# Performance work log

Hardware: AMD Instinct MI355X
Metric: run time of the kernel (lower is better)

The kernel has to match this reference:

```python
import math
import jax, jax.numpy as jnp
import numpy as np

B, C, T = 8, 512, 1024
H = 8
HD = C // H  # 64
CLIP = 4
COUT = 512


def setup_inputs() -> dict:
    key = jax.random.key(0)
    ks = jax.random.split(key, 12)
    s_qkv = math.sqrt(6.0 / (C + C))  # xavier_uniform for 1x1 conv
    queries = jax.random.normal(ks[0], (B, C, T), dtype=jnp.float32)
    Wq = jax.random.uniform(ks[1], (C, C), jnp.float32, -s_qkv, s_qkv)
    bq = jnp.zeros((C,), jnp.float32)
    Wk = jax.random.uniform(ks[2], (C, C), jnp.float32, -s_qkv, s_qkv)
    bk = jnp.zeros((C,), jnp.float32)
    Wv = jax.random.uniform(ks[3], (C, C), jnp.float32, -s_qkv, s_qkv)
    bv = jnp.zeros((C,), jnp.float32)
    Wp = jax.random.normal(ks[4], (COUT, C), jnp.float32) * (1.0 / math.sqrt(C))
    bp = jnp.zeros((COUT,), jnp.float32)
    w_std = HD ** (-0.5)
    wK = jax.random.normal(ks[5], (1, 2 * CLIP + 1, HD), jnp.float32) * w_std
    wV = jax.random.normal(ks[6], (1, 2 * CLIP + 1, HD), jnp.float32) * w_std
    return {"queries": queries, "Wq": Wq, "bq": bq, "Wk": Wk, "bk": bk,
            "Wv": Wv, "bv": bv, "Wp": Wp, "bp": bp, "wK": wK, "wV": wV}


def _get_relative_embedding(w, length):
    # w: [1, 2*CLIP+1, HD] -> [1, 2*length-1, HD]
    emb_len = 2 * length - 1
    p = max(emb_len - 2 * CLIP - 1, 0)
    pc, pf = (p + 1) // 2, p // 2  # ceil, floor of p/2
    w = jnp.pad(w, ((0, 0), (pc, pf), (0, 0)))
    idx = max(CLIP + 1 - length, 0)
    return w[:, idx:idx + emb_len]


def _rel_to_abs(x):
    # x: [B, H, L, 2L-1] -> [B, H, L, L]  (pad/shift trick)
    b, h, L, _ = x.shape
    x = jnp.pad(x, ((0, 0), (0, 0), (0, 0), (0, 1)))           # [b,h,L,2L]
    x = x.reshape(b, h, L * 2 * L)
    x = jnp.pad(x, ((0, 0), (0, 0), (0, L - 1)))
    x = x.reshape(b, h, L + 1, 2 * L - 1)
    return x[:, :, :L, L - 1:]


def _abs_to_rel(x):
    # x: [B, H, L, L] -> [B, H, L, 2L-1]
    b, h, L, _ = x.shape
    x = jnp.pad(x, ((0, 0), (0, 0), (0, 0), (0, L - 1)))       # [b,h,L,2L-1]
    x = x.reshape(b, h, L * (2 * L - 1))
    x = jnp.pad(x, ((0, 0), (0, 0), (L, 0)))
    x = x.reshape(b, h, L, 2 * L)
    return x[:, :, :, 1:]


def reference(queries, Wq, bq, Wk, bk, Wv, bv, Wp, bp, wK, wV):
    b, c, t = queries.shape
    scale = 1.0 / math.sqrt(HD)
    # 1x1-conv projections (self-attention: keys = values = queries)
    q = jnp.einsum('oc,bct->bot', Wq, queries) + bq[None, :, None]
    k = jnp.einsum('oc,bct->bot', Wk, queries) + bk[None, :, None]
    v = jnp.einsum('oc,bct->bot', Wv, queries) + bv[None, :, None]
    # [b, H, t, HD]
    q = q.reshape(b, H, HD, t).transpose(0, 1, 3, 2)
    k = k.reshape(b, H, HD, t).transpose(0, 1, 3, 2)
    v = v.reshape(b, H, HD, t).transpose(0, 1, 3, 2)
    scores = jnp.einsum('bhtd,bhsd->bhts', q, k) * scale
    # relative-position key bias
    rel_k = _get_relative_embedding(wK, t)[0]                  # [2t-1, HD]
    pos = jnp.einsum('bhtd,md->bhtm', q, rel_k)                # [b,H,t,2t-1]
    scores = scores + _rel_to_abs(pos) * scale
    alignments = jax.nn.softmax(scores, axis=-1)
    attn = jnp.einsum('bhts,bhsd->bhtd', alignments, v)
    # relative-position value bias
    rel_v = _get_relative_embedding(wV, t)[0]                  # [2t-1, HD]
    pos_rel = _abs_to_rel(alignments)                          # [b,H,t,2t-1]
    attn = attn + jnp.einsum('bhtm,md->bhtd', pos_rel, rel_v)
    attn = attn.transpose(0, 1, 3, 2).reshape(b, c, t)         # [b, C, t]
    out = jnp.einsum('oc,bct->bot', Wp, attn) + bp[None, :, None]
    return out, alignments
```

## Files before the change

### kernel.cpp

```cpp
#include <hip/hip_runtime.h>
#include <hip/hip_bf16.h>

#define BB 8
#define CC 512
#define TT 1024
#define HH 8
#define HD 64
#define CLIPW 4
#define NCOUT 512

using bf16 = __hip_bfloat16;
typedef __bf16 bf16x8_t __attribute__((ext_vector_type(8)));
typedef __bf16 bf16x4_t __attribute__((ext_vector_type(4)));
typedef float f32x4_t __attribute__((ext_vector_type(4)));

__global__ __launch_bounds__(256) void prep_w(
    const float* __restrict__ Wq, const float* __restrict__ Wk,
    const float* __restrict__ Wv, const float* __restrict__ Wp,
    bf16* __restrict__ wqf, bf16* __restrict__ wkf,
    bf16* __restrict__ wvf, bf16* __restrict__ wpf) {
  const int which = blockIdx.y;
  const float* W = (which == 0) ? Wq : (which == 1) ? Wk : (which == 2) ? Wv : Wp;
  bf16* F = (which == 0) ? wqf : (which == 1) ? wkf : (which == 2) ? wvf : wpf;
  const int gid = blockIdx.x * 256 + threadIdx.x;
  const int l = gid & 63;
  const int fid = gid >> 6;
  const int ct = fid & 15, ot = fid >> 4;
  const int sl = l & 15, g = l >> 4;
  const float* src = W + (size_t)(ot * 16 + sl) * CC + ct * 32 + g * 8;
  bf16x8_t p;
#pragma unroll
  for (int j = 0; j < 8; ++j) p[j] = (__bf16)src[j];
  *(bf16x8_t*)(F + (size_t)fid * 512 + l * 8) = p;
}

__global__ __launch_bounds__(256) void prep_x(
    const float* __restrict__ X, bf16* __restrict__ xfrag) {
  __shared__ float Xs[32][72];
  const int fi = blockIdx.x;
  const int b = fi & 7;
  const int k = fi >> 3;
  const int ct = k & 15, tq = k >> 4;
  const int c0 = ct * 32, t0 = tq * 64;
  const int tid = threadIdx.x;
  {
    const int ci = tid >> 4;
    const int t4 = (tid & 15) * 4;
#pragma unroll
    for (int cp = 0; cp < 2; ++cp) {
      const int c = cp * 16 + ci;
      const float4 x4 = *(const float4*)&X[((size_t)b * CC + c0 + c) * TT + t0 + t4];
      *(float4*)&Xs[c][t4] = x4;
    }
  }
  __syncthreads();
  const int l = tid & 63, fr = tid >> 6;
  const int sl = l & 15, g = l >> 4;
  bf16x8_t p;
#pragma unroll
  for (int j = 0; j < 8; ++j) p[j] = (__bf16)Xs[g * 8 + j][fr * 16 + sl];
  *(bf16x8_t*)(xfrag + (((size_t)b * 64 + tq * 4 + fr) * 16 + ct) * 512 + l * 8) = p;
}

__global__ __launch_bounds__(256) void gemm_qkv2(
    const bf16* __restrict__ xfrag,
    const bf16* __restrict__ wqf, const bf16* __restrict__ wkf,
    const bf16* __restrict__ wvf,
    const float* __restrict__ bq, const float* __restrict__ bk,
    const float* __restrict__ bv,
    bf16* __restrict__ qfrag, bf16* __restrict__ kfrag, bf16* __restrict__ vfrag) {
  __shared__ __align__(16) float Cs[64 * 68];
  const int fi = blockIdx.x;
  const int b  = fi & 7;
  const int k2 = fi >> 3;
  const int y  = k2 % 24;
  const int xb = k2 / 24;
  const int m  = y >> 3;
  const int o0 = (y & 7) * 64;
  const int t0 = xb * 64;
  const bf16* WF = (m == 0) ? wqf : (m == 1) ? wkf : wvf;
  const float* bias = (m == 0) ? bq : (m == 1) ? bk : bv;

  const int tid = threadIdx.x;
  const int w = tid >> 6, l = tid & 63, g = l >> 4, sl = l & 15;
  const int wr = w >> 1, wc = w & 1;
  const int ot0 = (o0 >> 4) + wr * 2;
  const int tt0 = (t0 >> 4) + wc * 2;

  f32x4_t acc[2][2] = {};
#pragma unroll 4
  for (int ct = 0; ct < 16; ++ct) {
    bf16x8_t a[2], bb[2];
#pragma unroll
    for (int mm = 0; mm < 2; ++mm)
      a[mm] = *(const bf16x8_t*)(WF + ((size_t)(ot0 + mm) * 16 + ct) * 512 + l * 8);
#pragma unroll
    for (int nn = 0; nn < 2; ++nn)
      bb[nn] = *(const bf16x8_t*)(xfrag + (((size_t)b * 64 + tt0 + nn) * 16 + ct) * 512 + l * 8);
#pragma unroll
    for (int mm = 0; mm < 2; ++mm)
#pragma unroll
      for (int nn = 0; nn < 2; ++nn)
        acc[mm][nn] = __builtin_amdgcn_mfma_f32_16x16x32_bf16(a[mm], bb[nn], acc[mm][nn], 0, 0, 0);
  }

#pragma unroll
  for (int mm = 0; mm < 2; ++mm)
#pragma unroll
    for (int nn = 0; nn < 2; ++nn)
#pragma unroll
      for (int r = 0; r < 4; ++r)
        Cs[(wr * 32 + mm * 16 + 4 * g + r) * 68 + wc * 32 + nn * 16 + sl] = acc[mm][nn][r];
  __syncthreads();

  const int hh2 = o0 >> 6;
  const int bh  = b * HH + hh2;
  const int fr = tid >> 6, l2 = tid & 63;
  const int sl2 = l2 & 15, g2 = l2 >> 4;
  if (m == 0) {
#pragma unroll
    for (int kh = 0; kh < 2; ++kh) {
      bf16x8_t p;
#pragma unroll
      for (int j = 0; j < 8; ++j) {
        const int d = kh * 32 + g2 * 8 + j;
        p[j] = (__bf16)(Cs[d * 68 + fr * 16 + sl2] + bias[o0 + d]);
      }
      *(bf16x8_t*)(qfrag + (((size_t)bh * 64 + (t0 >> 4) + fr) * 2 + kh) * 512 + l2 * 8) = p;
    }
  } else if (m == 1) {
    bf16* dpf = kfrag + (((size_t)bh * 64 + (t0 >> 4) + fr) * 2) * 512;
#pragma unroll
    for (int half = 0; half < 2; ++half) {
      bf16x8_t p;
#pragma unroll
      for (int j = 0; j < 8; ++j) {
        const int d = half * 32 + g2 * 8 + j;
        p[j] = (__bf16)(Cs[d * 68 + fr * 16 + sl2] + bias[o0 + d]);
      }
      *(bf16x8_t*)(dpf + half * 512 + l2 * 8) = p;
    }
  } else {
    const int dt = fr;
    const int d  = dt * 16 + sl2;
    const float bv_ = bias[o0 + d];
#pragma unroll
    for (int i2p = 0; i2p < 2; ++i2p) {
      const int i2 = (t0 >> 5) + i2p;
      bf16x8_t p;
#pragma unroll
      for (int j = 0; j < 8; ++j) {
        const int tloc = i2p * 32 + g2 * 8 + j;
        p[j] = (__bf16)(Cs[d * 68 + tloc] + bv_);
      }
      *(bf16x8_t*)(vfrag + ((((size_t)bh * 32 + i2) * 4 + dt) * 64 + l2) * 8) = p;
    }
  }
}

__global__ __launch_bounds__(256) void gemm_out2(
    const bf16* __restrict__ attnfrag, const bf16* __restrict__ wpf,
    const float* __restrict__ bp, float* __restrict__ out) {
  __shared__ __align__(16) float Cs[64 * 68];
  const int fi = blockIdx.x;
  const int b  = fi & 7;
  const int k2 = fi >> 3;
  const int o0 = (k2 & 7) * 64;
  const int t0 = (k2 >> 3) * 64;
  const int tid = threadIdx.x;
  const int w = tid >> 6, l = tid & 63, g = l >> 4, sl = l & 15;
  const int wr = w >> 1, wc = w & 1;
  const int ot0 = (o0 >> 4) + wr * 2;
  const int tt0 = (t0 >> 4) + wc * 2;

  f32x4_t acc[2][2] = {};
#pragma unroll 4
  for (int ct = 0; ct < 16; ++ct) {
    bf16x8_t a[2], bb[2];
#pragma unroll
    for (int mm = 0; mm < 2; ++mm)
      a[mm] = *(const bf16x8_t*)(wpf + ((size_t)(ot0 + mm) * 16 + ct) * 512 + l * 8);
#pragma unroll
    for (int nn = 0; nn < 2; ++nn)
      bb[nn] = *(const bf16x8_t*)(attnfrag + (((size_t)b * 64 + tt0 + nn) * 16 + ct) * 512 + l * 8);
#pragma unroll
    for (int mm = 0; mm < 2; ++mm)
#pragma unroll
      for (int nn = 0; nn < 2; ++nn)
        acc[mm][nn] = __builtin_amdgcn_mfma_f32_16x16x32_bf16(a[mm], bb[nn], acc[mm][nn], 0, 0, 0);
  }

#pragma unroll
  for (int mm = 0; mm < 2; ++mm)
#pragma unroll
    for (int nn = 0; nn < 2; ++nn)
#pragma unroll
      for (int r = 0; r < 4; ++r)
        Cs[(wr * 32 + mm * 16 + 4 * g + r) * 68 + wc * 32 + nn * 16 + sl] = acc[mm][nn][r];
  __syncthreads();

  const int o = tid >> 2, tq = tid & 3;
  const float bv_ = bp[o0 + o];
  float* dp = out + ((size_t)b * NCOUT + o0 + o) * TT + t0 + tq * 16;
#pragma unroll
  for (int i4 = 0; i4 < 4; ++i4) {
    f32x4_t v = *(const f32x4_t*)&Cs[o * 68 + tq * 16 + i4 * 4];
    v[0] += bv_; v[1] += bv_; v[2] += bv_; v[3] += bv_;
    *(f32x4_t*)(dp + i4 * 4) = v;
  }
}

__global__ __launch_bounds__(256, 4) void attn_v12(
    const bf16* __restrict__ qfrag, const bf16* __restrict__ kfrag,
    const bf16* __restrict__ vfrag,
    const float* __restrict__ wK, const float* __restrict__ wV,
    float* __restrict__ align_out, bf16* __restrict__ attnfrag) {
  const int fi   = blockIdx.x;
  const int xcd  = fi & 7;
  const int k2   = fi >> 3;
  const int bh   = ((k2 >> 6) << 3) + xcd;
  const int qblk = k2 & 63;
  const int b = bh >> 3, h = bh & 7;
  const int q0 = qblk * 16;

  const int tid = threadIdx.x;
  const int w = tid >> 6, l = tid & 63, g = l >> 4, ql = l & 15;
  const int qabs  = q0 + ql;
  const int sbase = w * 256;

  __shared__ __align__(16) char smem[39424];
  __bf16* eL    = (__bf16*)smem;
  float* bandv  = (float*)(smem + 33792);
  float* bandP  = (float*)(smem + 36864);
  float* redbuf = (float*)(smem + 39168);
  float* invL   = (float*)(smem + 33792);
  float* obuf   = (float*)smem;
  float* stg    = (float*)(smem + 17408);

  for (int i = tid; i < 576; i += 256) bandP[i] = 0.f;

  const bf16* qfb = qfrag + (((size_t)bh * 64 + (q0 >> 4)) * 2) * 512 + l * 8;
  const bf16x8_t qa0 = *(const bf16x8_t*)qfb;
  const bf16x8_t qa1 = *(const bf16x8_t*)(qfb + 512);

  {
    const int j = (ql < 9) ? ql : 0;
    const float* wkr = wK + j * HD + g * 8;
    const f32x4_t w0 = *(const f32x4_t*)wkr;
    const f32x4_t w1 = *(const f32x4_t*)(wkr + 4);
    const f32x4_t w2 = *(const f32x4_t*)(wkr + 32);
    const f32x4_t w3 = *(const f32x4_t*)(wkr + 36);
    bf16x8_t ka0, ka1;
#pragma unroll
    for (int i = 0; i < 4; ++i) {
      ka0[i] = (__bf16)w0[i]; ka0[4 + i] = (__bf16)w1[i];
      ka1[i] = (__bf16)w2[i]; ka1[4 + i] = (__bf16)w3[i];
    }
    f32x4_t bacc = {0.f, 0.f, 0.f, 0.f};
    bacc = __builtin_amdgcn_mfma_f32_16x16x32_bf16(ka0, qa0, bacc, 0, 0, 0);
    bacc = __builtin_amdgcn_mfma_f32_16x16x32_bf16(ka1, qa1, bacc, 0, 0, 0);
#pragma unroll
    for (int r = 0; r < 4; ++r)
      if (4 * g + r < 9) bandv[(w * 16 + ql) * 12 + 4 * g + r] = bacc[r];
  }

  float ls = 0.f;
  bf16x4_t stash[16];
  const int erow = (w * 16 + ql) * 264;
  const bf16* kfb = kfrag + (((size_t)bh * 64 + w * 16) * 2) * 512 + l * 8;
#pragma unroll
  for (int st = 0; st < 16; ++st) {
    const bf16x8_t k0 = *(const bf16x8_t*)(kfb + (size_t)st * 1024);
    const bf16x8_t k1 = *(const bf16x8_t*)(kfb + (size_t)st * 1024 + 512);
    f32x4_t a = {0.f, 0.f, 0.f, 0.f};
    a = __builtin_amdgcn_mfma_f32_16x16x32_bf16(k0, qa0, a, 0, 0, 0);
    a = __builtin_amdgcn_mfma_f32_16x16x32_bf16(k1, qa1, a, 0, 0, 0);
    const int s0t = sbase + st * 16;
    const bool near = (s0t + 15 >= q0 - CLIPW) && (s0t <= q0 + 15 + CLIPW);
#pragma unroll
    for (int r = 0; r < 4; ++r) {
      float x = a[r];
      if (near) {
        const int delta = s0t + 4 * g + r - qabs;
        if ((unsigned)(delta + CLIPW) <= 2 * CLIPW)
          x += bandv[(w * 16 + ql) * 12 + delta + CLIPW];
      }
      const float e = __expf(x * 0.125f);
      stash[st][r] = (__bf16)e;
      ls += e;
    }
    *(bf16x4_t*)&eL[erow + st * 16 + 4 * g] = stash[st];
  }
  ls += __shfl_xor(ls, 16);
  ls += __shfl_xor(ls, 32);
  if (l < 16) redbuf[w * 16 + ql] = ls;
  __syncthreads();
  const float inv = 1.0f / (redbuf[ql] + redbuf[16 + ql] + redbuf[32 + ql] + redbuf[48 + ql]);
  if (l < 16) invL[w * 16 + l] = inv;

#pragma unroll
  for (int st = 0; st < 16; ++st) {
    const int s0t = sbase + st * 16;
    const bool near = (s0t + 15 >= q0 - CLIPW) && (s0t <= q0 + 15 + CLIPW);
    if (near) {
#pragma unroll
      for (int r = 0; r < 4; ++r) {
        const int delta = s0t + 4 * g + r - qabs;
        if ((unsigned)(delta + CLIPW) <= 2 * CLIPW)
          bandP[ql * 36 + delta + CLIPW] = (float)stash[st][r] * inv;
      }
    }
  }

  f32x4_t oacc[4] = {};
  const bf16* vfb = vfrag + (((size_t)bh * 32 + w * 8) * 4) * 512 + l * 8;
  float* abase = align_out + ((size_t)bh * TT + q0) * TT + sbase + l * 4;
#pragma unroll
  for (int i2 = 0; i2 < 8; ++i2) {
    const bf16x8_t pb = *(const bf16x8_t*)&eL[erow + i2 * 32 + 8 * g];
#pragma unroll
    for (int dt = 0; dt < 4; ++dt) {
      const bf16x8_t va = *(const bf16x8_t*)(vfb + ((size_t)i2 * 4 + dt) * 512);
      oacc[dt] = __builtin_amdgcn_mfma_f32_16x16x32_bf16(va, pb, oacc[dt], 0, 0, 0);
    }
#pragma unroll
    for (int qq = 0; qq < 2; ++qq) {
      const int q = i2 * 2 + qq;
      const float iq = invL[w * 16 + q];
      const bf16x4_t e4 = *(const bf16x4_t*)&eL[(w * 16 + q) * 264 + l * 4];
      f32x4_t p4;
      p4[0] = (float)e4[0] * iq;
      p4[1] = (float)e4[1] * iq;
      p4[2] = (float)e4[2] * iq;
      p4[3] = (float)e4[3] * iq;
      __builtin_nontemporal_store(p4, (f32x4_t*)(abase + (size_t)q * TT));
    }
  }
#pragma unroll
  for (int dt = 0; dt < 4; ++dt) {
    oacc[dt][0] *= inv; oacc[dt][1] *= inv;
    oacc[dt][2] *= inv; oacc[dt][3] *= inv;
  }

  __syncthreads();

#pragma unroll
  for (int dt = 0; dt < 4; ++dt)
    *(f32x4_t*)&obuf[w * 1088 + ql * 68 + dt * 16 + 4 * g] = oacc[dt];
  __syncthreads();

  if (w == 0) {
    f32x4_t osum[4];
#pragma unroll
    for (int dt = 0; dt < 4; ++dt) {
      const int off = ql * 68 + dt * 16 + 4 * g;
      osum[dt] = *(const f32x4_t*)&obuf[off] + *(const f32x4_t*)&obuf[1088 + off] +
                 *(const f32x4_t*)&obuf[2176 + off] + *(const f32x4_t*)&obuf[3264 + off];
    }
    const f32x4_t b0 = *(const f32x4_t*)&bandP[ql * 36 + g * 8];
    const f32x4_t b1 = *(const f32x4_t*)&bandP[ql * 36 + g * 8 + 4];
    bf16x8_t pbb;
#pragma unroll
    for (int i = 0; i < 4; ++i) {
      pbb[i] = (__bf16)b0[i];
      pbb[4 + i] = (__bf16)b1[i];
    }
#pragma unroll
    for (int dt = 0; dt < 4; ++dt) {
      bf16x8_t wa;
#pragma unroll
      for (int jj = 0; jj < 8; ++jj) {
        const int j = g * 8 + jj;
        wa[jj] = (__bf16)((j < 9) ? wV[j * HD + dt * 16 + ql] : 0.f);
      }
      osum[dt] = __builtin_amdgcn_mfma_f32_16x16x32_bf16(wa, pbb, osum[dt], 0, 0, 0);
    }
#pragma unroll
    for (int dt = 0; dt < 4; ++dt)
#pragma unroll
      for (int r = 0; r < 4; ++r)
        stg[(dt * 16 + 4 * g + r) * 17 + ql] = osum[dt][r];
#pragma unroll
    for (int ctl = 0; ctl < 2; ++ctl) {
      bf16x8_t p;
#pragma unroll
      for (int j = 0; j < 8; ++j)
        p[j] = (__bf16)stg[(ctl * 32 + g * 8 + j) * 17 + ql];
      *(bf16x8_t*)(attnfrag +
                   (((size_t)b * 64 + (q0 >> 4)) * 16 + h * 2 + ctl) * 512 + l * 8) = p;
    }
  }
}

extern "C" void kernel_launch(void* const* d_in, const int* in_sizes, int n_in,
                              void* d_out, int out_size, void* d_ws, size_t ws_size,
                              hipStream_t stream) {
  const float* X  = (const float*)d_in[0];
  const float* Wq = (const float*)d_in[1];
  const float* bq = (const float*)d_in[2];
  const float* Wk = (const float*)d_in[3];
  const float* bk = (const float*)d_in[4];
  const float* Wv = (const float*)d_in[5];
  const float* bv = (const float*)d_in[6];
  const float* Wp = (const float*)d_in[7];
  const float* bp = (const float*)d_in[8];
  const float* wK = (const float*)d_in[9];
  const float* wV = (const float*)d_in[10];

  float* out       = (float*)d_out;
  float* align_out = out + (size_t)BB * NCOUT * TT;

  const size_t SZ = (size_t)BB * HH * TT * HD;
  const size_t WF = 512 * 512;
  bf16* qfrag    = (bf16*)d_ws;
  bf16* kfrag    = qfrag + SZ;
  bf16* vfrag    = qfrag + 2 * SZ;
  bf16* attnfrag = qfrag + 3 * SZ;
  bf16* xfrag    = qfrag + 4 * SZ;
  bf16* wqf      = qfrag + 5 * SZ;
  bf16* wkf      = wqf + WF;
  bf16* wvf      = wkf + WF;
  bf16* wpf      = wvf + WF;

  prep_w<<<dim3(128, 4), 256, 0, stream>>>(Wq, Wk, Wv, Wp, wqf, wkf, wvf, wpf);
  prep_x<<<dim3(2048), 256, 0, stream>>>(X, xfrag);
  gemm_qkv2<<<dim3(3072), 256, 0, stream>>>(
      xfrag, wqf, wkf, wvf, bq, bk, bv, qfrag, kfrag, vfrag);
  attn_v12<<<dim3(4096), 256, 0, stream>>>(
      qfrag, kfrag, vfrag, wK, wV, align_out, attnfrag);
  gemm_out2<<<dim3(1024), 256, 0, stream>>>(attnfrag, wpf, bp, out);
}
```

Baseline: 143.0 us.

## Split attention key range across eight waves per block instead of four

The attention kernel now runs 512 threads per block. Each of the eight waves handles 128 keys instead of 256, which halves the per-wave stash and the LDS row stride. The softmax denominator is reduced over eight partial sums, and the P·V partial outputs are combined in two phases through shared memory. Alignment stores now have each half-wave write a different query row. This adds parallelism and latency hiding per block, at the cost of an extra barrier and possibly lower occupancy under the 512-thread launch bound.

```diff
diff --git a/kernel.cpp b/kernel.cpp
--- a/kernel.cpp
+++ b/kernel.cpp
@@ -12,6 +12,7 @@
 using bf16 = __hip_bfloat16;
 typedef __bf16 bf16x8_t __attribute__((ext_vector_type(8)));
 typedef __bf16 bf16x4_t __attribute__((ext_vector_type(4)));
+typedef __bf16 bf16x2_t __attribute__((ext_vector_type(2)));
 typedef float f32x4_t __attribute__((ext_vector_type(4)));
 
 __global__ __launch_bounds__(256) void prep_w(
@@ -210,7 +211,7 @@
   }
 }
 
-__global__ __launch_bounds__(256, 4) void attn_v12(
+__global__ __launch_bounds__(512, 4) void attn_v16(
     const bf16* __restrict__ qfrag, const bf16* __restrict__ kfrag,
     const bf16* __restrict__ vfrag,
     const float* __restrict__ wK, const float* __restrict__ wV,
@@ -226,18 +227,18 @@
   const int tid = threadIdx.x;
   const int w = tid >> 6, l = tid & 63, g = l >> 4, ql = l & 15;
   const int qabs  = q0 + ql;
-  const int sbase = w * 256;
-
-  __shared__ __align__(16) char smem[39424];
-  __bf16* eL    = (__bf16*)smem;
-  float* bandv  = (float*)(smem + 33792);
-  float* bandP  = (float*)(smem + 36864);
-  float* redbuf = (float*)(smem + 39168);
-  float* invL   = (float*)(smem + 33792);
-  float* obuf   = (float*)smem;
-  float* stg    = (float*)(smem + 17408);
-
-  for (int i = tid; i < 576; i += 256) bandP[i] = 0.f;
+  const int sbase = w * 128;
+
+  __shared__ __align__(16) char smem[37440];
+  __bf16* eL      = (__bf16*)smem;
+  float* obuf     = (float*)smem;
+  float* stg      = (float*)(smem + 17408);
+  float* bandv16  = (float*)(smem + 33792);
+  float* bandP    = (float*)(smem + 34560);
+  float* redbuf   = (float*)(smem + 36864);
+  float* invL     = (float*)(smem + 37376);
+
+  for (int i = tid; i < 576; i += 512) bandP[i] = 0.f;
 
   const bf16* qfb = qfrag + (((size_t)bh * 64 + (q0 >> 4)) * 2) * 512 + l * 8;
   const bf16x8_t qa0 = *(const bf16x8_t*)qfb;
@@ -261,15 +262,15 @@
     bacc = __builtin_amdgcn_mfma_f32_16x16x32_bf16(ka1, qa1, bacc, 0, 0, 0);
 #pragma unroll
     for (int r = 0; r < 4; ++r)
-      if (4 * g + r < 9) bandv[(w * 16 + ql) * 12 + 4 * g + r] = bacc[r];
+      if (4 * g + r < 9) bandv16[ql * 12 + 4 * g + r] = bacc[r];
   }
 
   float ls = 0.f;
-  bf16x4_t stash[16];
-  const int erow = (w * 16 + ql) * 264;
-  const bf16* kfb = kfrag + (((size_t)bh * 64 + w * 16) * 2) * 512 + l * 8;
-#pragma unroll
-  for (int st = 0; st < 16; ++st) {
+  bf16x4_t stash[8];
+  const int erow = (w * 16 + ql) * 132;
+  const bf16* kfb = kfrag + (((size_t)bh * 64 + w * 8) * 2) * 512 + l * 8;
+#pragma unroll
+  for (int st = 0; st < 8; ++st) {
     const bf16x8_t k0 = *(const bf16x8_t*)(kfb + (size_t)st * 1024);
     const bf16x8_t k1 = *(const bf16x8_t*)(kfb + (size_t)st * 1024 + 512);
     f32x4_t a = {0.f, 0.f, 0.f, 0.f};
@@ -283,7 +284,7 @@
       if (near) {
         const int delta = s0t + 4 * g + r - qabs;
         if ((unsigned)(delta + CLIPW) <= 2 * CLIPW)
-          x += bandv[(w * 16 + ql) * 12 + delta + CLIPW];
+          x += bandv16[ql * 12 + delta + CLIPW];
       }
       const float e = __expf(x * 0.125f);
       stash[st][r] = (__bf16)e;
@@ -295,11 +296,14 @@
   ls += __shfl_xor(ls, 32);
   if (l < 16) redbuf[w * 16 + ql] = ls;
   __syncthreads();
-  const float inv = 1.0f / (redbuf[ql] + redbuf[16 + ql] + redbuf[32 + ql] + redbuf[48 + ql]);
-  if (l < 16) invL[w * 16 + l] = inv;
-
-#pragma unroll
-  for (int st = 0; st < 16; ++st) {
+  float lsum = 0.f;
+#pragma unroll
+  for (int k = 0; k < 8; ++k) lsum += redbuf[k * 16 + ql];
+  const float inv = 1.0f / lsum;
+  if (l < 16) invL[l] = inv;
+
+#pragma unroll
+  for (int st = 0; st < 8; ++st) {
     const int s0t = sbase + st * 16;
     const bool near = (s0t + 15 >= q0 - CLIPW) && (s0t <= q0 + 15 + CLIPW);
     if (near) {
@@ -313,27 +317,29 @@
   }
 
   f32x4_t oacc[4] = {};
-  const bf16* vfb = vfrag + (((size_t)bh * 32 + w * 8) * 4) * 512 + l * 8;
-  float* abase = align_out + ((size_t)bh * TT + q0) * TT + sbase + l * 4;
-#pragma unroll
-  for (int i2 = 0; i2 < 8; ++i2) {
-    const bf16x8_t pb = *(const bf16x8_t*)&eL[erow + i2 * 32 + 8 * g];
+  const bf16* vfb = vfrag + (((size_t)bh * 32 + w * 4) * 4) * 512 + l * 8;
+  const int lh = l >> 5;
+  const int l32 = l & 31;
+  float* abase = align_out + ((size_t)bh * TT + q0) * TT + sbase;
+#pragma unroll
+  for (int i2l = 0; i2l < 4; ++i2l) {
+    const bf16x8_t pb = *(const bf16x8_t*)&eL[erow + i2l * 32 + 8 * g];
 #pragma unroll
     for (int dt = 0; dt < 4; ++dt) {
-      const bf16x8_t va = *(const bf16x8_t*)(vfb + ((size_t)i2 * 4 + dt) * 512);
+      const bf16x8_t va = *(const bf16x8_t*)(vfb + ((size_t)i2l * 4 + dt) * 512);
       oacc[dt] = __builtin_amdgcn_mfma_f32_16x16x32_bf16(va, pb, oacc[dt], 0, 0, 0);
     }
 #pragma unroll
     for (int qq = 0; qq < 2; ++qq) {
-      const int q = i2 * 2 + qq;
-      const float iq = invL[w * 16 + q];
-      const bf16x4_t e4 = *(const bf16x4_t*)&eL[(w * 16 + q) * 264 + l * 4];
+      const int q = i2l * 4 + qq * 2 + lh;
+      const float iq = invL[q];
+      const bf16x4_t e4 = *(const bf16x4_t*)&eL[(w * 16 + q) * 132 + l32 * 4];
       f32x4_t p4;
       p4[0] = (float)e4[0] * iq;
       p4[1] = (float)e4[1] * iq;
       p4[2] = (float)e4[2] * iq;
       p4[3] = (float)e4[3] * iq;
-      __builtin_nontemporal_store(p4, (f32x4_t*)(abase + (size_t)q * TT));
+      __builtin_nontemporal_store(p4, (f32x4_t*)(abase + (size_t)q * TT + l32 * 4));
     }
   }
 #pragma unroll
@@ -343,10 +349,20 @@
   }
 
   __syncthreads();
-
-#pragma unroll
-  for (int dt = 0; dt < 4; ++dt)
-    *(f32x4_t*)&obuf[w * 1088 + ql * 68 + dt * 16 + 4 * g] = oacc[dt];
+  if (w < 4) {
+#pragma unroll
+    for (int dt = 0; dt < 4; ++dt)
+      *(f32x4_t*)&obuf[w * 1088 + ql * 68 + dt * 16 + 4 * g] = oacc[dt];
+  }
+  __syncthreads();
+  if (w >= 4) {
+#pragma unroll
+    for (int dt = 0; dt < 4; ++dt) {
+      f32x4_t cur = *(const f32x4_t*)&obuf[(w - 4) * 1088 + ql * 68 + dt * 16 + 4 * g];
+      cur += oacc[dt];
+      *(f32x4_t*)&obuf[(w - 4) * 1088 + ql * 68 + dt * 16 + 4 * g] = cur;
+    }
+  }
   __syncthreads();
 
   if (w == 0) {
@@ -426,7 +442,7 @@
   prep_x<<<dim3(2048), 256, 0, stream>>>(X, xfrag);
   gemm_qkv2<<<dim3(3072), 256, 0, stream>>>(
       xfrag, wqf, wkf, wvf, bq, bk, bv, qfrag, kfrag, vfrag);
-  attn_v12<<<dim3(4096), 256, 0, stream>>>(
+  attn_v16<<<dim3(4096), 512, 0, stream>>>(
       qfrag, kfrag, vfrag, wK, wV, align_out, attnfrag);
   gemm_out2<<<dim3(1024), 256, 0, stream>>>(attnfrag, wpf, bp, out);
 }
```

Result: slower. 146.7 us (+2.6%).
